# Kernel optimization log

Measured on AMD Instinct MI355X. Metric: run time of the kernel, lower is better.

The kernel has to match this reference:

```python
import jax, jax.numpy as jnp
import numpy as np

NUM_NODES = 32768  # B*N = 16*2048
NUM_REL = 10
NUM_BASES = 4
D = 256
E = 524288


def _rgcn_layer(x, src, dst, rel, basis, comp, root, bias):
    """Basis-decomposed relational GCN layer with per-relation mean aggregation.
    x: [N, Din], basis: [NB, Din, Dout], comp: [R, NB], root: [Din, Dout], bias: [Dout].
    """
    n = x.shape[0]
    # project all nodes through each basis once: [N, NB, Dout]
    xb = jnp.einsum('ni,bio->nbo', x, basis)
    coeff = comp[rel]  # [E, NB] per-edge basis coefficients
    # mean normalization per (destination node, relation) pair
    seg = rel * n + dst  # combined segment id, [E]
    cnt = jax.ops.segment_sum(jnp.ones(rel.shape[0], x.dtype), seg,
                              num_segments=NUM_REL * n)
    inv = jnp.where(cnt > 0, 1.0 / cnt, 0.0)[seg]  # [E]
    # per-edge message: sum_b coeff[e,b] * xb[src_e, b, :] (loop over small NB)
    msg = jnp.zeros((rel.shape[0], basis.shape[2]), x.dtype)
    for b in range(basis.shape[0]):
        msg = msg + coeff[:, b:b + 1] * xb[src, b]
    msg = msg * inv[:, None]
    agg = jax.ops.segment_sum(msg, dst, num_segments=n)  # [N, Dout]
    return agg + x @ root + bias


def setup_inputs() -> dict:
    key = jax.random.key(0)
    ks = jax.random.split(key, 16)
    p = lambda k, shp: (jax.random.normal(k, shp, jnp.float32) * 0.05)
    inp = {
        'x': jax.random.normal(ks[0], (16, 2048, D), jnp.float32),
        't': jax.random.randint(ks[1], (16,), 0, 1000),
        'obj_cond': jax.random.randint(ks[2], (16, 2048), 0, 160),
        'edge_cond': jax.random.randint(ks[3], (2, E), 0, NUM_NODES),
        'relation_cond': jax.random.randint(ks[4], (E,), 0, NUM_REL),
        # layer 0: 256 -> 256 (hidden)
        'basis0': p(ks[5], (NUM_BASES, D, D)),
        'comp0': p(ks[6], (NUM_REL, NUM_BASES)),
        'root0': p(ks[7], (D, D)),
        'bias0': p(ks[8], (D,)),
        # layer 1: 256 -> 256 (output)
        'basis1': p(ks[9], (NUM_BASES, D, D)),
        'comp1': p(ks[10], (NUM_REL, NUM_BASES)),
        'root1': p(ks[11], (D, D)),
        'bias1': p(ks[12], (D,)),
    }
    return inp


def reference(x, t, obj_cond, edge_cond, relation_cond,
              basis0, comp0, root0, bias0, basis1, comp1, root1, bias1):
    B, N, Dm = x.shape
    h = x.reshape(B * N, Dm)
    src, dst = edge_cond[0], edge_cond[1]
    h = _rgcn_layer(h, src, dst, relation_cond, basis0, comp0, root0, bias0)
    h = jax.nn.relu(h)  # hidden-layer activation (dropout disabled at eval)
    h = _rgcn_layer(h, src, dst, relation_cond, basis1, comp1, root1, bias1)
    return h.reshape(B, N, Dm)
```

## Files before the change

### kernel.cpp

```cpp
#include <hip/hip_runtime.h>
#include <stdint.h>

#define NNODES 32768
#define NREL 10
#define NBASES 4
#define DIM 256
#define NEDGE 524288
#define KW 1280
#define KBASE 1024

#define HB 2048
#define CB 8192
#define WB 80

typedef __attribute__((ext_vector_type(8))) short bf16x8;
typedef __attribute__((ext_vector_type(4))) float f32x4;

__device__ __forceinline__ float bf2f(unsigned short u){
  union { unsigned int i; float f; } v; v.i = ((unsigned int)u) << 16; return v.f;
}
__device__ __forceinline__ unsigned short f2bf(float f){
  union { float f; unsigned int i; } v; v.f = f;
  unsigned int x = v.i;
  unsigned int r = (x + 0x7FFFu + ((x >> 16) & 1u)) >> 16;
  return (unsigned short)r;
}
__device__ __forceinline__ void gll16(const void* g, void* l){
  __builtin_amdgcn_global_load_lds((const __attribute__((address_space(1))) void*)g,
                                   (__attribute__((address_space(3))) void*)l, 16, 0, 0);
}

__global__ __launch_bounds__(256) void mega_prep(
    const int* __restrict__ ec, const int* __restrict__ rel,
    int* __restrict__ cnt_rd,
    const float* __restrict__ x, unsigned short* __restrict__ Xh,
    const float* __restrict__ basis0, const float* __restrict__ root0,
    unsigned short* __restrict__ Wt0,
    const float* __restrict__ basis1, const float* __restrict__ root1,
    unsigned short* __restrict__ Wt1)
{
  __shared__ float tile[64][65];
  int bid = blockIdx.x;
  int t = threadIdx.x;
  if (bid < HB){
    int e = bid * 256 + t;
    int d = ec[NEDGE + e];
    int r = rel[e];
    atomicAdd(&cnt_rd[(r << 15) + d], 1);
  } else if (bid < HB + CB){
    int i = (bid - HB) * 256 + t;
    float4 v = ((const float4*)x)[i];
    ushort4 o; o.x = f2bf(v.x); o.y = f2bf(v.y); o.z = f2bf(v.z); o.w = f2bf(v.w);
    ((ushort4*)Xh)[i] = o;
  } else {
    int b = bid - HB - CB;
    int layer = b / WB; b %= WB;
    const float* basis = layer ? basis1 : basis0;
    const float* root  = layer ? root1  : root0;
    unsigned short* Wt = layer ? Wt1    : Wt0;
    int k0 = (b % 20) * 64;
    int n0 = (b / 20) * 64;
    int tn = t & 63, tk = t >> 6;
#pragma unroll
    for (int i = 0; i < 64; i += 4){
      int k = k0 + tk + i;
      float v = (k < KBASE) ? basis[(size_t)k * 256 + n0 + tn]
                            : root[(size_t)(k - KBASE) * 256 + n0 + tn];
      tile[tk + i][tn] = v;
    }
    __syncthreads();
#pragma unroll
    for (int i = 0; i < 64; i += 4){
      int n = n0 + tk + i;
      Wt[(size_t)n * KW + k0 + tn] = f2bf(tile[tn][tk + i]);
    }
  }
}

__global__ __launch_bounds__(1024) void scan1(const int* __restrict__ cnt_rd,
                                              int* __restrict__ offs, int* __restrict__ blksum)
{
  __shared__ int sh[1024];
  int tid = threadIdx.x; int gid = blockIdx.x * 1024 + tid;
  int v = 0;
#pragma unroll
  for (int r = 0; r < NREL; r++) v += cnt_rd[(r << 15) + gid];
  sh[tid] = v; __syncthreads();
  for (int off = 1; off < 1024; off <<= 1){
    int t = (tid >= off) ? sh[tid - off] : 0;
    __syncthreads(); sh[tid] += t; __syncthreads();
  }
  offs[gid] = sh[tid] - v;
  if (tid == 1023) blksum[blockIdx.x] = sh[1023];
}
__global__ __launch_bounds__(64) void scan2(int* __restrict__ blksum)
{
  __shared__ int sh[64];
  int tid = threadIdx.x;
  int v = (tid < NNODES / 1024) ? blksum[tid] : 0;
  sh[tid] = v; __syncthreads();
  for (int off = 1; off < 64; off <<= 1){
    int t = (tid >= off) ? sh[tid - off] : 0;
    __syncthreads(); sh[tid] += t; __syncthreads();
  }
  if (tid < NNODES / 1024) blksum[tid] = sh[tid] - v;
}
__global__ __launch_bounds__(1024) void scan3(int* __restrict__ offs, const int* __restrict__ blksum)
{
  int gid = blockIdx.x * 1024 + threadIdx.x;
  offs[gid] += blksum[blockIdx.x];
  if (gid == 0) offs[NNODES] = NEDGE;
}

__global__ void scatter_kernel(const int* __restrict__ ec, const int* __restrict__ rel,
                               const int* __restrict__ offs, int* __restrict__ cursor,
                               unsigned int* __restrict__ meta)
{
  int e = blockIdx.x * 256 + threadIdx.x;
  int s = ec[e];
  int d = ec[NEDGE + e];
  int r = rel[e];
  int p = offs[d] + atomicAdd(&cursor[d], 1);
  meta[p] = ((unsigned int)s << 4) | (unsigned int)r;
}

__global__ __launch_bounds__(256) void agg5(
    const unsigned short* __restrict__ Xin,
    const int* __restrict__ offs,
    const unsigned int* __restrict__ meta,
    const float* __restrict__ comp,
    const int* __restrict__ cnt_rd,
    unsigned short* __restrict__ z)
{
  __shared__ __attribute__((aligned(16))) float wtab[4][40];
  int t = threadIdx.x;
  int wv = t >> 6, lane = t & 63;
  int d = blockIdx.x * 4 + wv;
  if (lane < 40){
    int r = lane >> 2, b = lane & 3;
    int cnt = cnt_rd[(r << 15) + d];
    wtab[wv][lane] = (cnt > 0) ? comp[r * NBASES + b] / (float)cnt : 0.0f;
  }
  __syncthreads();

  int col = lane * 4;
  const float4* wt4 = (const float4*)&wtab[wv][0];

  float acc[NBASES][4] = {};
  int e0 = offs[d], e1 = offs[d + 1];
  int e = e0;
  for (; e + 3 < e1; e += 4){
    unsigned int m0 = meta[e], m1 = meta[e + 1], m2 = meta[e + 2], m3 = meta[e + 3];
    float4 w0 = wt4[m0 & 15u], w1 = wt4[m1 & 15u], w2 = wt4[m2 & 15u], w3 = wt4[m3 & 15u];
    ushort4 v0 = *(const ushort4*)(Xin + ((size_t)(m0 >> 4)) * 256 + col);
    ushort4 v1 = *(const ushort4*)(Xin + ((size_t)(m1 >> 4)) * 256 + col);
    ushort4 v2 = *(const ushort4*)(Xin + ((size_t)(m2 >> 4)) * 256 + col);
    ushort4 v3 = *(const ushort4*)(Xin + ((size_t)(m3 >> 4)) * 256 + col);
#pragma unroll
    for (int b = 0; b < NBASES; b++){
      float a0 = ((const float*)&w0)[b];
      float a1 = ((const float*)&w1)[b];
      float a2 = ((const float*)&w2)[b];
      float a3 = ((const float*)&w3)[b];
      acc[b][0] += a0 * bf2f(v0.x) + a1 * bf2f(v1.x) + a2 * bf2f(v2.x) + a3 * bf2f(v3.x);
      acc[b][1] += a0 * bf2f(v0.y) + a1 * bf2f(v1.y) + a2 * bf2f(v2.y) + a3 * bf2f(v3.y);
      acc[b][2] += a0 * bf2f(v0.z) + a1 * bf2f(v1.z) + a2 * bf2f(v2.z) + a3 * bf2f(v3.z);
      acc[b][3] += a0 * bf2f(v0.w) + a1 * bf2f(v1.w) + a2 * bf2f(v2.w) + a3 * bf2f(v3.w);
    }
  }
  for (; e < e1; ++e){
    unsigned int md = meta[e];
    float4 w = wt4[md & 15u];
    ushort4 v = *(const ushort4*)(Xin + ((size_t)(md >> 4)) * 256 + col);
#pragma unroll
    for (int b = 0; b < NBASES; b++){
      float a = ((const float*)&w)[b];
      acc[b][0] += a * bf2f(v.x); acc[b][1] += a * bf2f(v.y);
      acc[b][2] += a * bf2f(v.z); acc[b][3] += a * bf2f(v.w);
    }
  }
#pragma unroll
  for (int b = 0; b < NBASES; b++){
    ushort4 o;
    o.x = f2bf(acc[b][0]); o.y = f2bf(acc[b][1]);
    o.z = f2bf(acc[b][2]); o.w = f2bf(acc[b][3]);
    *(ushort4*)(z + (size_t)d * KBASE + b * 256 + col) = o;
  }
}

__global__ __launch_bounds__(256) void gemm4(
    const unsigned short* __restrict__ A0,
    const unsigned short* __restrict__ A1,
    const unsigned short* __restrict__ Wt,
    const float* __restrict__ bias,
    unsigned short* __restrict__ outh,
    float* __restrict__ outf,
    int mode)
{
  __shared__ __attribute__((aligned(16))) short As[64 * 32];
  __shared__ __attribute__((aligned(16))) short Bs[256 * 32];
  int tid  = threadIdx.x;
  int m0   = blockIdx.x * 64;
  int lane = tid & 63;
  int wn   = tid >> 6;
  int lq = lane >> 4, lr = lane & 15;

  f32x4 zero = {0.f, 0.f, 0.f, 0.f};
  f32x4 acc[4][4];
#pragma unroll
  for (int i = 0; i < 4; i++)
#pragma unroll
    for (int j = 0; j < 4; j++) acc[i][j] = zero;

  int arow = tid >> 2;
  int akc  = ((tid & 3) - (tid >> 3)) & 3;

  for (int k0 = 0; k0 < KW; k0 += 32){
    __syncthreads();
    {
      const unsigned short* ga;
      if (k0 < KBASE) ga = A0 + (size_t)(m0 + arow) * KBASE + k0 + akc * 8;
      else            ga = A1 + (size_t)(m0 + arow) * 256 + (k0 - KBASE) + akc * 8;
      gll16(ga, As + tid * 8);
    }
#pragma unroll
    for (int i = 0; i < 4; i++){
      int gb  = tid + i * 256;
      int row = gb >> 2;
      int kc  = ((gb & 3) - (gb >> 3)) & 3;
      gll16(Wt + (size_t)row * KW + k0 + kc * 8, Bs + gb * 8);
    }
    __syncthreads();

    bf16x8 af[4], bfr[4];
#pragma unroll
    for (int i = 0; i < 4; i++){
      int row = i * 16 + lr;
      af[i] = *(const bf16x8*)(As + row * 32 + (((lq + (row >> 1)) & 3) * 8));
    }
#pragma unroll
    for (int j = 0; j < 4; j++){
      int row = wn * 64 + j * 16 + lr;
      bfr[j] = *(const bf16x8*)(Bs + row * 32 + (((lq + (row >> 1)) & 3) * 8));
    }
#pragma unroll
    for (int i = 0; i < 4; i++)
#pragma unroll
      for (int j = 0; j < 4; j++)
        acc[i][j] = __builtin_amdgcn_mfma_f32_16x16x32_bf16(af[i], bfr[j], acc[i][j], 0, 0, 0);
  }

#pragma unroll
  for (int i = 0; i < 4; i++)
#pragma unroll
    for (int j = 0; j < 4; j++)
#pragma unroll
      for (int r = 0; r < 4; r++){
        int gm = m0 + i * 16 + lq * 4 + r;
        int gn = wn * 64 + j * 16 + lr;
        float v = acc[i][j][r] + bias[gn];
        size_t idx = (size_t)gm * 256 + gn;
        if (mode == 1) outh[idx] = f2bf(fmaxf(v, 0.f));
        else           outf[idx] = v;
      }
}

extern "C" void kernel_launch(void* const* d_in, const int* in_sizes, int n_in,
                              void* d_out, int out_size, void* d_ws, size_t ws_size,
                              hipStream_t stream)
{
  const float* x      = (const float*)d_in[0];
  const int*   ec     = (const int*)d_in[3];
  const int*   rel    = (const int*)d_in[4];
  const float* basis0 = (const float*)d_in[5];
  const float* comp0  = (const float*)d_in[6];
  const float* root0  = (const float*)d_in[7];
  const float* bias0  = (const float*)d_in[8];
  const float* basis1 = (const float*)d_in[9];
  const float* comp1  = (const float*)d_in[10];
  const float* root1  = (const float*)d_in[11];
  const float* bias1  = (const float*)d_in[12];

  char* p = (char*)d_ws;
  unsigned short* z   = (unsigned short*)p; p += (size_t)NNODES * KBASE * 2;
  unsigned short* Xh  = (unsigned short*)p; p += (size_t)NNODES * DIM * 2;
  unsigned short* h   = (unsigned short*)p; p += (size_t)NNODES * DIM * 2;
  unsigned short* Wt0 = (unsigned short*)p; p += (size_t)256 * KW * 2;
  unsigned short* Wt1 = (unsigned short*)p; p += (size_t)256 * KW * 2;
  unsigned int* meta  = (unsigned int*)p;   p += (size_t)NEDGE * 4;
  int* cnt_rd  = (int*)p;   p += (size_t)NREL * NNODES * 4;
  int* cursor  = (int*)p;   p += (size_t)NNODES * 4;
  int* offs    = (int*)p;   p += (size_t)(NNODES + 1) * 4;
  int* blksum  = (int*)p;   p += 1024;

  hipMemsetAsync(cnt_rd, 0, ((size_t)NREL * NNODES + (size_t)NNODES) * 4, stream);

  mega_prep<<<HB + CB + 2 * WB, 256, 0, stream>>>(
      ec, rel, cnt_rd, x, Xh, basis0, root0, Wt0, basis1, root1, Wt1);

  scan1<<<NNODES / 1024, 1024, 0, stream>>>(cnt_rd, offs, blksum);
  scan2<<<1, 64, 0, stream>>>(blksum);
  scan3<<<NNODES / 1024, 1024, 0, stream>>>(offs, blksum);
  scatter_kernel<<<NEDGE / 256, 256, 0, stream>>>(ec, rel, offs, cursor, meta);

  agg5<<<NNODES / 4, 256, 0, stream>>>(Xh, offs, meta, comp0, cnt_rd, z);
  gemm4<<<NNODES / 64, 256, 0, stream>>>(z, Xh, Wt0, bias0, h, nullptr, 1);

  agg5<<<NNODES / 4, 256, 0, stream>>>(h, offs, meta, comp1, cnt_rd, z);
  gemm4<<<NNODES / 64, 256, 0, stream>>>(z, h, Wt1, bias1, nullptr, (float*)d_out, 2);
}
```

Baseline: 330.1 us.

## Fuse edge aggregation with basis GEMM via shared-memory z tile

Merges the per-node aggregation kernel and the MFMA GEMM into one kernel that builds a 32-row bf16 z tile in LDS and consumes it directly, removing the large global z intermediate. Also folds the second scan pass into the add-offset pass by summing block totals serially. The trade-off is a smaller GEMM tile, more weight reloads, and higher LDS use that limits occupancy during the latency-bound gather phase.

```diff
diff --git a/kernel.cpp b/kernel.cpp
--- a/kernel.cpp
+++ b/kernel.cpp
@@ -93,22 +93,14 @@
   offs[gid] = sh[tid] - v;
   if (tid == 1023) blksum[blockIdx.x] = sh[1023];
 }
-__global__ __launch_bounds__(64) void scan2(int* __restrict__ blksum)
-{
-  __shared__ int sh[64];
-  int tid = threadIdx.x;
-  int v = (tid < NNODES / 1024) ? blksum[tid] : 0;
-  sh[tid] = v; __syncthreads();
-  for (int off = 1; off < 64; off <<= 1){
-    int t = (tid >= off) ? sh[tid - off] : 0;
-    __syncthreads(); sh[tid] += t; __syncthreads();
-  }
-  if (tid < NNODES / 1024) blksum[tid] = sh[tid] - v;
-}
-__global__ __launch_bounds__(1024) void scan3(int* __restrict__ offs, const int* __restrict__ blksum)
-{
-  int gid = blockIdx.x * 1024 + threadIdx.x;
-  offs[gid] += blksum[blockIdx.x];
+__global__ __launch_bounds__(1024) void scan3b(int* __restrict__ offs,
+                                               const int* __restrict__ blksum)
+{
+  int bid = blockIdx.x;
+  int pre = 0;
+  for (int i = 0; i < bid; i++) pre += blksum[i];
+  int gid = bid * 1024 + threadIdx.x;
+  offs[gid] += pre;
   if (gid == 0) offs[NNODES] = NEDGE;
 }
 
@@ -124,119 +116,117 @@
   meta[p] = ((unsigned int)s << 4) | (unsigned int)r;
 }
 
-__global__ __launch_bounds__(256) void agg5(
+__global__ __launch_bounds__(256) void fused_layer(
     const unsigned short* __restrict__ Xin,
     const int* __restrict__ offs,
     const unsigned int* __restrict__ meta,
     const float* __restrict__ comp,
     const int* __restrict__ cnt_rd,
-    unsigned short* __restrict__ z)
-{
-  __shared__ __attribute__((aligned(16))) float wtab[4][40];
-  int t = threadIdx.x;
-  int wv = t >> 6, lane = t & 63;
-  int d = blockIdx.x * 4 + wv;
-  if (lane < 40){
-    int r = lane >> 2, b = lane & 3;
-    int cnt = cnt_rd[(r << 15) + d];
-    wtab[wv][lane] = (cnt > 0) ? comp[r * NBASES + b] / (float)cnt : 0.0f;
-  }
-  __syncthreads();
-
-  int col = lane * 4;
-  const float4* wt4 = (const float4*)&wtab[wv][0];
-
-  float acc[NBASES][4] = {};
-  int e0 = offs[d], e1 = offs[d + 1];
-  int e = e0;
-  for (; e + 3 < e1; e += 4){
-    unsigned int m0 = meta[e], m1 = meta[e + 1], m2 = meta[e + 2], m3 = meta[e + 3];
-    float4 w0 = wt4[m0 & 15u], w1 = wt4[m1 & 15u], w2 = wt4[m2 & 15u], w3 = wt4[m3 & 15u];
-    ushort4 v0 = *(const ushort4*)(Xin + ((size_t)(m0 >> 4)) * 256 + col);
-    ushort4 v1 = *(const ushort4*)(Xin + ((size_t)(m1 >> 4)) * 256 + col);
-    ushort4 v2 = *(const ushort4*)(Xin + ((size_t)(m2 >> 4)) * 256 + col);
-    ushort4 v3 = *(const ushort4*)(Xin + ((size_t)(m3 >> 4)) * 256 + col);
-#pragma unroll
-    for (int b = 0; b < NBASES; b++){
-      float a0 = ((const float*)&w0)[b];
-      float a1 = ((const float*)&w1)[b];
-      float a2 = ((const float*)&w2)[b];
-      float a3 = ((const float*)&w3)[b];
-      acc[b][0] += a0 * bf2f(v0.x) + a1 * bf2f(v1.x) + a2 * bf2f(v2.x) + a3 * bf2f(v3.x);
-      acc[b][1] += a0 * bf2f(v0.y) + a1 * bf2f(v1.y) + a2 * bf2f(v2.y) + a3 * bf2f(v3.y);
-      acc[b][2] += a0 * bf2f(v0.z) + a1 * bf2f(v1.z) + a2 * bf2f(v2.z) + a3 * bf2f(v3.z);
-      acc[b][3] += a0 * bf2f(v0.w) + a1 * bf2f(v1.w) + a2 * bf2f(v2.w) + a3 * bf2f(v3.w);
-    }
-  }
-  for (; e < e1; ++e){
-    unsigned int md = meta[e];
-    float4 w = wt4[md & 15u];
-    ushort4 v = *(const ushort4*)(Xin + ((size_t)(md >> 4)) * 256 + col);
-#pragma unroll
-    for (int b = 0; b < NBASES; b++){
-      float a = ((const float*)&w)[b];
-      acc[b][0] += a * bf2f(v.x); acc[b][1] += a * bf2f(v.y);
-      acc[b][2] += a * bf2f(v.z); acc[b][3] += a * bf2f(v.w);
-    }
-  }
-#pragma unroll
-  for (int b = 0; b < NBASES; b++){
-    ushort4 o;
-    o.x = f2bf(acc[b][0]); o.y = f2bf(acc[b][1]);
-    o.z = f2bf(acc[b][2]); o.w = f2bf(acc[b][3]);
-    *(ushort4*)(z + (size_t)d * KBASE + b * 256 + col) = o;
-  }
-}
-
-__global__ __launch_bounds__(256) void gemm4(
-    const unsigned short* __restrict__ A0,
-    const unsigned short* __restrict__ A1,
     const unsigned short* __restrict__ Wt,
     const float* __restrict__ bias,
     unsigned short* __restrict__ outh,
     float* __restrict__ outf,
     int mode)
 {
-  __shared__ __attribute__((aligned(16))) short As[64 * 32];
+  __shared__ __attribute__((aligned(16))) short ztile[32 * 1024];
   __shared__ __attribute__((aligned(16))) short Bs[256 * 32];
-  int tid  = threadIdx.x;
-  int m0   = blockIdx.x * 64;
-  int lane = tid & 63;
-  int wn   = tid >> 6;
+  float* wtab = (float*)Bs;
+
+  int tid = threadIdx.x;
+  int m0  = blockIdx.x * 32;
+  int wv = tid >> 6, lane = tid & 63;
+
+  for (int idx = tid; idx < 32 * 40; idx += 256){
+    int dl = idx / 40, j = idx - dl * 40;
+    int r = j >> 2, b = j & 3;
+    int cnt = cnt_rd[(r << 15) + m0 + dl];
+    wtab[idx] = (cnt > 0) ? comp[j] / (float)cnt : 0.0f;
+  }
+  __syncthreads();
+
+  int col = lane * 4;
+  for (int i = 0; i < 8; i++){
+    int rloc = wv * 8 + i;
+    int d = m0 + rloc;
+    const float4* wt4 = (const float4*)(wtab + rloc * 40);
+    float acc[NBASES][4] = {};
+    int e0 = offs[d], e1 = offs[d + 1];
+    int e = e0;
+    for (; e + 3 < e1; e += 4){
+      unsigned int md0 = meta[e], md1 = meta[e + 1], md2 = meta[e + 2], md3 = meta[e + 3];
+      float4 w0 = wt4[md0 & 15u], w1 = wt4[md1 & 15u], w2 = wt4[md2 & 15u], w3 = wt4[md3 & 15u];
+      ushort4 v0 = *(const ushort4*)(Xin + ((size_t)(md0 >> 4)) * 256 + col);
+      ushort4 v1 = *(const ushort4*)(Xin + ((size_t)(md1 >> 4)) * 256 + col);
+      ushort4 v2 = *(const ushort4*)(Xin + ((size_t)(md2 >> 4)) * 256 + col);
+      ushort4 v3 = *(const ushort4*)(Xin + ((size_t)(md3 >> 4)) * 256 + col);
+#pragma unroll
+      for (int b = 0; b < NBASES; b++){
+        float a0 = ((const float*)&w0)[b];
+        float a1 = ((const float*)&w1)[b];
+        float a2 = ((const float*)&w2)[b];
+        float a3 = ((const float*)&w3)[b];
+        acc[b][0] += a0 * bf2f(v0.x) + a1 * bf2f(v1.x) + a2 * bf2f(v2.x) + a3 * bf2f(v3.x);
+        acc[b][1] += a0 * bf2f(v0.y) + a1 * bf2f(v1.y) + a2 * bf2f(v2.y) + a3 * bf2f(v3.y);
+        acc[b][2] += a0 * bf2f(v0.z) + a1 * bf2f(v1.z) + a2 * bf2f(v2.z) + a3 * bf2f(v3.z);
+        acc[b][3] += a0 * bf2f(v0.w) + a1 * bf2f(v1.w) + a2 * bf2f(v2.w) + a3 * bf2f(v3.w);
+      }
+    }
+    for (; e < e1; ++e){
+      unsigned int md = meta[e];
+      float4 w = wt4[md & 15u];
+      ushort4 v = *(const ushort4*)(Xin + ((size_t)(md >> 4)) * 256 + col);
+#pragma unroll
+      for (int b = 0; b < NBASES; b++){
+        float a = ((const float*)&w)[b];
+        acc[b][0] += a * bf2f(v.x); acc[b][1] += a * bf2f(v.y);
+        acc[b][2] += a * bf2f(v.z); acc[b][3] += a * bf2f(v.w);
+      }
+    }
+#pragma unroll
+    for (int b = 0; b < NBASES; b++){
+      int gr = b * 32 + (lane >> 1);
+      int slot = (gr + rloc) & 127;
+      ushort4 o;
+      o.x = f2bf(acc[b][0]); o.y = f2bf(acc[b][1]);
+      o.z = f2bf(acc[b][2]); o.w = f2bf(acc[b][3]);
+      *(ushort4*)(ztile + rloc * 1024 + slot * 8 + (lane & 1) * 4) = o;
+    }
+  }
+
+  int wn = wv;
   int lq = lane >> 4, lr = lane & 15;
-
   f32x4 zero = {0.f, 0.f, 0.f, 0.f};
-  f32x4 acc[4][4];
-#pragma unroll
-  for (int i = 0; i < 4; i++)
-#pragma unroll
-    for (int j = 0; j < 4; j++) acc[i][j] = zero;
-
-  int arow = tid >> 2;
-  int akc  = ((tid & 3) - (tid >> 3)) & 3;
+  f32x4 cacc[2][4];
+#pragma unroll
+  for (int i = 0; i < 2; i++)
+#pragma unroll
+    for (int j = 0; j < 4; j++) cacc[i][j] = zero;
 
   for (int k0 = 0; k0 < KW; k0 += 32){
     __syncthreads();
-    {
-      const unsigned short* ga;
-      if (k0 < KBASE) ga = A0 + (size_t)(m0 + arow) * KBASE + k0 + akc * 8;
-      else            ga = A1 + (size_t)(m0 + arow) * 256 + (k0 - KBASE) + akc * 8;
-      gll16(ga, As + tid * 8);
-    }
 #pragma unroll
     for (int i = 0; i < 4; i++){
-      int gb  = tid + i * 256;
-      int row = gb >> 2;
-      int kc  = ((gb & 3) - (gb >> 3)) & 3;
-      gll16(Wt + (size_t)row * KW + k0 + kc * 8, Bs + gb * 8);
+      int g   = tid + i * 256;
+      int row = g >> 2;
+      int kc  = ((g & 3) - (g >> 3)) & 3;
+      gll16(Wt + (size_t)row * KW + k0 + kc * 8, Bs + g * 8);
     }
     __syncthreads();
 
-    bf16x8 af[4], bfr[4];
-#pragma unroll
-    for (int i = 0; i < 4; i++){
-      int row = i * 16 + lr;
-      af[i] = *(const bf16x8*)(As + row * 32 + (((lq + (row >> 1)) & 3) * 8));
+    bf16x8 af[2], bfr[4];
+    if (k0 < KBASE){
+#pragma unroll
+      for (int i = 0; i < 2; i++){
+        int row = i * 16 + lr;
+        int slot = ((k0 >> 3) + lq + row) & 127;
+        af[i] = *(const bf16x8*)(ztile + row * 1024 + slot * 8);
+      }
+    } else {
+#pragma unroll
+      for (int i = 0; i < 2; i++){
+        int row = i * 16 + lr;
+        af[i] = *(const bf16x8*)(Xin + (size_t)(m0 + row) * 256 + (k0 - KBASE) + lq * 8);
+      }
     }
 #pragma unroll
     for (int j = 0; j < 4; j++){
@@ -244,21 +234,21 @@
       bfr[j] = *(const bf16x8*)(Bs + row * 32 + (((lq + (row >> 1)) & 3) * 8));
     }
 #pragma unroll
-    for (int i = 0; i < 4; i++)
+    for (int i = 0; i < 2; i++)
 #pragma unroll
       for (int j = 0; j < 4; j++)
-        acc[i][j] = __builtin_amdgcn_mfma_f32_16x16x32_bf16(af[i], bfr[j], acc[i][j], 0, 0, 0);
-  }
-
-#pragma unroll
-  for (int i = 0; i < 4; i++)
+        cacc[i][j] = __builtin_amdgcn_mfma_f32_16x16x32_bf16(af[i], bfr[j], cacc[i][j], 0, 0, 0);
+  }
+
+#pragma unroll
+  for (int i = 0; i < 2; i++)
 #pragma unroll
     for (int j = 0; j < 4; j++)
 #pragma unroll
       for (int r = 0; r < 4; r++){
         int gm = m0 + i * 16 + lq * 4 + r;
         int gn = wn * 64 + j * 16 + lr;
-        float v = acc[i][j][r] + bias[gn];
+        float v = cacc[i][j][r] + bias[gn];
         size_t idx = (size_t)gm * 256 + gn;
         if (mode == 1) outh[idx] = f2bf(fmaxf(v, 0.f));
         else           outf[idx] = v;
@@ -282,7 +272,6 @@
   const float* bias1  = (const float*)d_in[12];
 
   char* p = (char*)d_ws;
-  unsigned short* z   = (unsigned short*)p; p += (size_t)NNODES * KBASE * 2;
   unsigned short* Xh  = (unsigned short*)p; p += (size_t)NNODES * DIM * 2;
   unsigned short* h   = (unsigned short*)p; p += (size_t)NNODES * DIM * 2;
   unsigned short* Wt0 = (unsigned short*)p; p += (size_t)256 * KW * 2;
@@ -299,13 +288,11 @@
       ec, rel, cnt_rd, x, Xh, basis0, root0, Wt0, basis1, root1, Wt1);
 
   scan1<<<NNODES / 1024, 1024, 0, stream>>>(cnt_rd, offs, blksum);
-  scan2<<<1, 64, 0, stream>>>(blksum);
-  scan3<<<NNODES / 1024, 1024, 0, stream>>>(offs, blksum);
+  scan3b<<<NNODES / 1024, 1024, 0, stream>>>(offs, blksum);
   scatter_kernel<<<NEDGE / 256, 256, 0, stream>>>(ec, rel, offs, cursor, meta);
 
-  agg5<<<NNODES / 4, 256, 0, stream>>>(Xh, offs, meta, comp0, cnt_rd, z);
-  gemm4<<<NNODES / 64, 256, 0, stream>>>(z, Xh, Wt0, bias0, h, nullptr, 1);
-
-  agg5<<<NNODES / 4, 256, 0, stream>>>(h, offs, meta, comp1, cnt_rd, z);
-  gemm4<<<NNODES / 64, 256, 0, stream>>>(z, h, Wt1, bias1, nullptr, (float*)d_out, 2);
-}
+  fused_layer<<<NNODES / 32, 256, 0, stream>>>(Xh, offs, meta, comp0, cnt_rd,
+                                               Wt0, bias0, h, nullptr, 1);
+  fused_layer<<<NNODES / 32, 256, 0, stream>>>(h, offs, meta, comp1, cnt_rd,
+                                               Wt1, bias1, nullptr, (float*)d_out, 2);
+}
```

Measured after the change: 441.9 us. 1.34x slower.
